# Performance work log

Hardware: AMD Instinct MI355X
Metric: run time of the kernel (lower is better)

The kernel has to match this reference:

```python
import jax, jax.numpy as jnp
import numpy as np

B, C, H, W = 16, 256, 64, 64


def _conv1x1(x, w, b):
    # x: [B,C,H,W], w: [O,C], b: [O]
    return jnp.einsum('oc,bchw->bohw', w, x) + b[None, :, None, None]


def _maxpool2(x):
    b, c, h, w = x.shape
    return x.reshape(b, c, h // 2, 2, w // 2, 2).max(axis=(3, 5))


def setup_inputs() -> dict:
    key = jax.random.key(0)
    ks = jax.random.split(key, 10)
    c8, c2 = C // 8, C // 2
    s = lambda fan_in: 1.0 / np.sqrt(fan_in)
    return {
        'x': jax.random.normal(ks[0], (B, C, H, W), dtype=jnp.float32),
        'query_w': jax.random.normal(ks[1], (c8, C), dtype=jnp.float32) * s(C),
        'query_b': jnp.zeros((c8,), dtype=jnp.float32),
        'key_w': jax.random.normal(ks[2], (c8, C), dtype=jnp.float32) * s(C),
        'key_b': jnp.zeros((c8,), dtype=jnp.float32),
        'val_w': jax.random.normal(ks[3], (c2, C), dtype=jnp.float32) * s(C),
        'val_b': jnp.zeros((c2,), dtype=jnp.float32),
        'val2_w': jax.random.normal(ks[4], (C, c2), dtype=jnp.float32) * s(c2),
        'val2_b': jnp.zeros((C,), dtype=jnp.float32),
        'gamma': jnp.zeros((1,), dtype=jnp.float32) + 0.5,  # nonzero so attention path contributes
    }


def reference(x, query_w, query_b, key_w, key_b, val_w, val_b, val2_w, val2_b, gamma):
    b, nc, h, w = x.shape
    loc = h * w
    down = loc // 4
    c8, c2 = nc // 8, nc // 2

    # query: conv then raw view to [B, HW, C//8] (NOT a permute; faithful to torch .view)
    q = _conv1x1(x, query_w, query_b)              # [B, C/8, H, W]
    q = q.reshape(b, loc, c8)                      # raw reshape, mixes channel/spatial

    # key: conv -> 2x2 maxpool -> raw view -> permute(0,2,1)
    k = _maxpool2(_conv1x1(x, key_w, key_b))       # [B, C/8, H/2, W/2]
    k = k.reshape(b, down, c8).transpose(0, 2, 1)  # [B, C/8, down]

    # value: conv -> 2x2 maxpool -> raw view
    v = _maxpool2(_conv1x1(x, val_w, val_b))       # [B, C/2, H/2, W/2]
    v = v.reshape(b, down, c2)                     # [B, down, C/2]

    attn = jnp.einsum('bqd,bdk->bqk', q, k)        # [B, HW, down], no 1/sqrt(d)
    attn_weights = jax.nn.softmax(attn, axis=1)    # softmax over QUERY axis (dim=1), as in source
    applied = jnp.einsum('bqk,bkc->bqc', attn_weights, v)  # [B, HW, C/2]

    # raw view back to [B, C/2, w, h] (note w,h swapped in source)
    applied = applied.reshape(b, c2, w, h)
    out = _conv1x1(applied, val2_w, val2_b)        # [B, C, w, h]
    return gamma * out + x
```

## Files before the change

### kernel.cpp

```cpp
#include <hip/hip_runtime.h>
#include <hip/hip_bf16.h>


typedef short s8v __attribute__((ext_vector_type(8)));
typedef float f4v __attribute__((ext_vector_type(4)));
typedef unsigned short u16v8 __attribute__((ext_vector_type(8)));
typedef unsigned short u16v4 __attribute__((ext_vector_type(4)));

#define MFMA16(a, b, c) __builtin_amdgcn_mfma_f32_16x16x32_bf16((a), (b), (c), 0, 0, 0)
#define LOG2E 1.4426950408889634f
#define EXP2 __builtin_amdgcn_exp2f

__device__ __forceinline__ unsigned short f2b(float f) {
    __hip_bfloat16 h = __float2bfloat16(f);
    return *reinterpret_cast<unsigned short*>(&h);
}
__device__ __forceinline__ float b2f(unsigned short u) {
    union { unsigned int i; float f; } v; v.i = ((unsigned int)u) << 16; return v.f;
}

__global__ void prep_weights(const float* __restrict__ qw, const float* __restrict__ qb,
                             const float* __restrict__ kw, const float* __restrict__ kb,
                             const float* __restrict__ vw, const float* __restrict__ vb,
                             const float* __restrict__ v2w,
                             unsigned short* __restrict__ wqkv, float* __restrict__ bias,
                             unsigned short* __restrict__ w2b) {
    int i = blockIdx.x * 256 + threadIdx.x;
    if (i < 49152) {
        int r = i >> 8, c = i & 255; float v;
        if (r < 32)       v = qw[r * 256 + c];
        else if (r < 64)  v = kw[(r - 32) * 256 + c] * LOG2E;
        else              v = vw[(r - 64) * 256 + c];
        wqkv[i] = f2b(v);
    } else if (i < 49152 + 32768) {
        int k = i - 49152; w2b[k] = f2b(v2w[k]);
    } else if (i < 49152 + 32768 + 192) {
        int r = i - 49152 - 32768;
        bias[r] = (r < 32) ? qb[r] : (r < 64 ? kb[r - 32] * LOG2E : vb[r - 64]);
    }
}

__global__ __launch_bounds__(256) void qkv_pool(const unsigned short* __restrict__ wqkv,
                                                const float* __restrict__ bias,
                                                const float* __restrict__ x,
                                                unsigned short* __restrict__ qf,
                                                unsigned short* __restrict__ kf,
                                                unsigned short* __restrict__ vf) {
    __shared__ alignas(16) unsigned short xt[32768];
    int b = blockIdx.y, r = blockIdx.x;
    int p0 = r * 128;
    int t = threadIdx.x;
    int wave = t >> 6, lane = t & 63;
    int m = lane & 15, quad = lane >> 4;
    const float* xb = x + (size_t)b * 1048576;

    {
        int pq = t & 31, kb = t >> 5;
        #pragma unroll
        for (int s = 0; s < 8; ++s) {
            int kbase = s * 32 + kb * 4;
            float4 f0 = *(const float4*)(xb + (size_t)(kbase + 0) * 4096 + p0 + pq * 4);
            float4 f1 = *(const float4*)(xb + (size_t)(kbase + 1) * 4096 + p0 + pq * 4);
            float4 f2 = *(const float4*)(xb + (size_t)(kbase + 2) * 4096 + p0 + pq * 4);
            float4 f3 = *(const float4*)(xb + (size_t)(kbase + 3) * 4096 + p0 + pq * 4);
            int ko = kbase >> 3, sub = kbase & 7;
            #pragma unroll
            for (int pi = 0; pi < 4; ++pi) {
                int p = pq * 4 + pi;
                float a0 = pi == 0 ? f0.x : pi == 1 ? f0.y : pi == 2 ? f0.z : f0.w;
                float a1 = pi == 0 ? f1.x : pi == 1 ? f1.y : pi == 2 ? f1.z : f1.w;
                float a2 = pi == 0 ? f2.x : pi == 1 ? f2.y : pi == 2 ? f2.z : f2.w;
                float a3 = pi == 0 ? f3.x : pi == 1 ? f3.y : pi == 2 ? f3.z : f3.w;
                u16v4 pk; pk[0] = f2b(a0); pk[1] = f2b(a1); pk[2] = f2b(a2); pk[3] = f2b(a3);
                int swz = (p & 7) ^ ((p >> 2) & 7);
                *(u16v4*)(&xt[p * 256 + ((ko ^ swz) << 3) + sub]) = pk;
            }
        }
    }
    __syncthreads();

    f4v acc[3][8] = {};
    for (int ks = 0; ks < 8; ++ks) {
        int k0 = ks * 32 + quad * 8;
        s8v afr[3];
        for (int mt = 0; mt < 3; ++mt)
            afr[mt] = *(const s8v*)(wqkv + (wave * 48 + mt * 16 + m) * 256 + k0);
        for (int nt = 0; nt < 8; ++nt) {
            int p = nt * 16 + m;
            int swz = (p & 7) ^ ((p >> 2) & 7);
            s8v bfr = *(const s8v*)(&xt[p * 256 + (((ks * 4 + quad) ^ swz) << 3)]);
            for (int mt = 0; mt < 3; ++mt)
                acc[mt][nt] = MFMA16(afr[mt], bfr, acc[mt][nt]);
        }
    }
    for (int mt = 0; mt < 3; ++mt) {
        int obase = wave * 48 + mt * 16;
        if (obase < 32) {
            for (int reg = 0; reg < 4; ++reg) {
                int o = obase + quad * 4 + reg;
                float bi = bias[o];
                for (int nt = 0; nt < 8; ++nt)
                    qf[(size_t)b * 131072 + (size_t)o * 4096 + p0 + nt * 16 + m] =
                        f2b(acc[mt][nt][reg] + bi);
            }
        } else {
            for (int reg = 0; reg < 4; ++reg) {
                int o = obase + quad * 4 + reg;
                float bi = bias[o];
                for (int nt = 0; nt < 4; ++nt) {
                    float vv = fmaxf(acc[mt][nt][reg], acc[mt][nt + 4][reg]);
                    float ov = __shfl_xor(vv, 1);
                    if ((m & 1) == 0) {
                        float res = fmaxf(vv, ov) + bi;
                        int w2 = nt * 8 + (m >> 1);
                        int sp = r * 32 + w2;
                        if (o < 64) kf[(size_t)b * 32768 + (size_t)(o - 32) * 1024 + sp] = f2b(res);
                        else        vf[(size_t)b * 131072 + (size_t)(o - 64) * 1024 + sp] = f2b(res);
                    }
                }
            }
        }
    }
}

__global__ __launch_bounds__(256) void col_stats(const unsigned short* __restrict__ qf,
                                                 const unsigned short* __restrict__ kf,
                                                 float* __restrict__ rs) {
    __shared__ float red[4][32];
    int b = blockIdx.y, j0 = blockIdx.x * 32;
    int wave = threadIdx.x >> 6, lane = threadIdx.x & 63;
    int m = lane & 15, quad = lane >> 4;
    const unsigned short* qb = qf + (size_t)b * 131072;
    f4v zero = {0.f, 0.f, 0.f, 0.f};

    s8v kfr0 = *(const s8v*)(kf + (size_t)b * 32768 + (size_t)(j0 + m) * 32 + quad * 8);
    s8v kfr1 = *(const s8v*)(kf + (size_t)b * 32768 + (size_t)(j0 + 16 + m) * 32 + quad * 8);

    float sm0 = 0.f, sm1 = 0.f;
    for (int it = wave; it < 256; it += 4) {
        s8v afr = *(const s8v*)(qb + (size_t)(it * 16 + m) * 32 + quad * 8);
        f4v s0 = MFMA16(afr, kfr0, zero);
        f4v s1 = MFMA16(afr, kfr1, zero);
        sm0 += (EXP2(s0[0]) + EXP2(s0[1])) + (EXP2(s0[2]) + EXP2(s0[3]));
        sm1 += (EXP2(s1[0]) + EXP2(s1[1])) + (EXP2(s1[2]) + EXP2(s1[3]));
    }
    sm0 += __shfl_xor(sm0, 16); sm0 += __shfl_xor(sm0, 32);
    sm1 += __shfl_xor(sm1, 16); sm1 += __shfl_xor(sm1, 32);
    if (lane < 16) { red[wave][m] = sm0; red[wave][16 + m] = sm1; }
    __syncthreads();
    if (threadIdx.x < 32) {
        float S = (red[0][threadIdx.x] + red[1][threadIdx.x]) +
                  (red[2][threadIdx.x] + red[3][threadIdx.x]);
        rs[b * 1024 + j0 + threadIdx.x] = 1.0f / S;
    }
}

__global__ __launch_bounds__(256) void transpose_scale_v(const unsigned short* __restrict__ src,
                                                         const float* __restrict__ rs,
                                                         unsigned short* __restrict__ dst) {
    __shared__ float tile[64][65];
    int b = blockIdx.z;
    size_t base = (size_t)b * 131072;
    int r0 = blockIdx.x * 64, c0 = blockIdx.y * 64;
    int tr = threadIdx.x >> 6, tc = threadIdx.x & 63;
    float scale = rs[b * 1024 + r0 + tc];
    for (int i = 0; i < 16; ++i) {
        int rl = i * 4 + tr;
        tile[rl][tc] = b2f(src[base + (size_t)(r0 + rl) * 128 + c0 + tc]);
    }
    __syncthreads();
    for (int i = 0; i < 16; ++i) {
        int cl = i * 4 + tr;
        int c = c0 + cl;
        int j = r0 + tc;
        int jc = j >> 7, jl = j & 127, g = jl >> 3, e = jl & 7;
        dst[base + jc * 16384 + c * 128 + ((g ^ (c & 7)) << 3) + e] =
            f2b(tile[tc][cl] * scale);
    }
}

__global__ __launch_bounds__(512, 4) void attn_fused(const unsigned short* __restrict__ qf,
                                                     const unsigned short* __restrict__ kf,
                                                     const unsigned short* __restrict__ vsw,
                                                     unsigned short* __restrict__ fa) {
    __shared__ alignas(16) unsigned short VS[16384];
    __shared__ alignas(16) unsigned short PT[16384];
    int lin = blockIdx.x + (blockIdx.y << 5);
    int b = lin & 15, l0 = (lin >> 4) << 7;
    int tid = threadIdx.x;
    int wave = tid >> 6, lane = tid & 63;
    int m = lane & 15, quad = lane >> 4;
    int ls = wave * 16;
    const unsigned short* qb = qf + (size_t)b * 131072;
    const unsigned short* kb = kf + (size_t)b * 32768;
    const unsigned short* vb = vsw + (size_t)b * 131072;

    s8v qa = *(const s8v*)(qb + (size_t)(l0 + ls + m) * 32 + quad * 8);
    f4v acc[8] = {};
    f4v zero = {0.f, 0.f, 0.f, 0.f};

    for (int jc = 0; jc < 8; ++jc) {
        const unsigned short* src = vb + jc * 16384 + tid * 8;
        u16v8 t0 = *(const u16v8*)(src);
        u16v8 t1 = *(const u16v8*)(src + 4096);
        u16v8 t2 = *(const u16v8*)(src + 8192);
        u16v8 t3 = *(const u16v8*)(src + 12288);

        int j0 = jc * 128;
        int l = ls + m;
        for (int jt = 0; jt < 8; ++jt) {
            s8v kfr = *(const s8v*)(kb + (size_t)(j0 + jt * 16 + m) * 32 + quad * 8);
            f4v st = MFMA16(kfr, qa, zero);
            unsigned int u0 = ((unsigned)f2b(EXP2(st[1])) << 16) |
                              (unsigned)f2b(EXP2(st[0]));
            unsigned int u1 = ((unsigned)f2b(EXP2(st[3])) << 16) |
                              (unsigned)f2b(EXP2(st[2]));
            int g = jt * 2 + (quad >> 1);
            int sub = (quad & 1) * 4;
            uint2 uu; uu.x = u0; uu.y = u1;
            *(uint2*)(&PT[l * 128 + ((g ^ (l & 7)) << 3) + sub]) = uu;
        }

        __syncthreads();

        {
            unsigned short* dstl = VS + tid * 8;
            *(u16v8*)(dstl)         = t0;
            *(u16v8*)(dstl + 4096)  = t1;
            *(u16v8*)(dstl + 8192)  = t2;
            *(u16v8*)(dstl + 12288) = t3;
        }

        __syncthreads();

        __builtin_amdgcn_s_setprio(1);
        for (int ks = 0; ks < 4; ++ks) {
            int gp = ks * 4 + quad;
            s8v pa = *(const s8v*)(&PT[l * 128 + ((gp ^ (l & 7)) << 3)]);
            for (int ct = 0; ct < 8; ++ct) {
                int c = ct * 16 + m;
                s8v vfr = *(const s8v*)(&VS[c * 128 + ((gp ^ (c & 7)) << 3)]);
                acc[ct] = MFMA16(pa, vfr, acc[ct]);
            }
        }
        __builtin_amdgcn_s_setprio(0);
    }
    for (int ct = 0; ct < 8; ++ct)
        for (int reg = 0; reg < 4; ++reg) {
            int l = l0 + ls + quad * 4 + reg;
            fa[(size_t)b * 524288 + (size_t)l * 128 + ct * 16 + m] = f2b(acc[ct][reg]);
        }
}

__global__ __launch_bounds__(256, 4) void final_gemm(const unsigned short* __restrict__ w2b,
                                                     const float* __restrict__ v2b,
                                                     const float* __restrict__ gamma,
                                                     const unsigned short* __restrict__ fa,
                                                     const float* __restrict__ x,
                                                     float* __restrict__ out) {
    __shared__ alignas(16) unsigned short gt[64][136];
    int b = blockIdx.z, bx = blockIdx.x;
    int p0 = bx * 64;
    int page = bx >> 1;
    int c0 = (bx & 1) * 64;
    int wave = threadIdx.x >> 6, lane = threadIdx.x & 63;
    int m = lane & 15, quad = lane >> 4;
    int obase = blockIdx.y * 128 + wave * 32;

    int row  = threadIdx.x >> 1;
    int half = threadIdx.x & 1;
    const unsigned short* fr = fa + (size_t)b * 524288 +
                               (size_t)(row * 32 + page) * 128 + c0 + half * 32;
    u16v8 t0 = *(const u16v8*)(fr);
    u16v8 t1 = *(const u16v8*)(fr + 8);
    u16v8 t2 = *(const u16v8*)(fr + 16);
    u16v8 t3 = *(const u16v8*)(fr + 24);

    float4 xv[2][4];
    #pragma unroll
    for (int mt = 0; mt < 2; ++mt) {
        size_t xrow = (size_t)b * 1048576 + (size_t)(obase + mt * 16 + m) * 4096;
        #pragma unroll
        for (int nt = 0; nt < 4; ++nt)
            xv[mt][nt] = *(const float4*)(x + xrow + p0 + nt * 16 + quad * 4);
    }

    {
        int pb = half * 32;
        #pragma unroll
        for (int i = 0; i < 8; ++i) {
            gt[pb + i][row]      = t0[i];
            gt[pb + 8 + i][row]  = t1[i];
            gt[pb + 16 + i][row] = t2[i];
            gt[pb + 24 + i][row] = t3[i];
        }
    }
    __syncthreads();

    f4v acc[2][4] = {};
    for (int ks = 0; ks < 4; ++ks) {
        int k0 = ks * 32 + quad * 8;
        s8v afr[2], bfr[4];
        #pragma unroll
        for (int mt = 0; mt < 2; ++mt)
            afr[mt] = *(const s8v*)(w2b + (obase + mt * 16 + m) * 128 + k0);
        #pragma unroll
        for (int nt = 0; nt < 4; ++nt)
            bfr[nt] = *(const s8v*)(&gt[nt * 16 + m][k0]);
        #pragma unroll
        for (int mt = 0; mt < 2; ++mt)
            #pragma unroll
            for (int nt = 0; nt < 4; ++nt)
                acc[mt][nt] = MFMA16(bfr[nt], afr[mt], acc[mt][nt]);
    }
    float g = gamma[0];
    #pragma unroll
    for (int mt = 0; mt < 2; ++mt) {
        int o = obase + mt * 16 + m;
        float bi = v2b[o];
        size_t xrow = (size_t)b * 1048576 + (size_t)o * 4096;
        #pragma unroll
        for (int nt = 0; nt < 4; ++nt) {
            size_t xi = xrow + p0 + nt * 16 + quad * 4;
            float4 ov;
            ov.x = g * (acc[mt][nt][0] + bi) + xv[mt][nt].x;
            ov.y = g * (acc[mt][nt][1] + bi) + xv[mt][nt].y;
            ov.z = g * (acc[mt][nt][2] + bi) + xv[mt][nt].z;
            ov.w = g * (acc[mt][nt][3] + bi) + xv[mt][nt].w;
            *(float4*)(out + xi) = ov;
        }
    }
}

extern "C" void kernel_launch(void* const* d_in, const int* in_sizes, int n_in,
                              void* d_out, int out_size, void* d_ws, size_t ws_size,
                              hipStream_t stream) {
    const float* x    = (const float*)d_in[0];
    const float* qw   = (const float*)d_in[1];
    const float* qb   = (const float*)d_in[2];
    const float* kw   = (const float*)d_in[3];
    const float* kb   = (const float*)d_in[4];
    const float* vw   = (const float*)d_in[5];
    const float* vb   = (const float*)d_in[6];
    const float* v2w  = (const float*)d_in[7];
    const float* v2b  = (const float*)d_in[8];
    const float* gamma = (const float*)d_in[9];
    float* out = (float*)d_out;

    char* ws = (char*)d_ws;
    size_t off = 0;
    auto alloc = [&](size_t bytes) { size_t o = off; off = (off + bytes + 255) & ~(size_t)255; return o; };
    unsigned short* wqkv = (unsigned short*)(ws + alloc(192 * 256 * 2));
    unsigned short* w2b  = (unsigned short*)(ws + alloc(256 * 128 * 2));
    float*          bias = (float*)(ws + alloc(192 * 4));
    float*          rs   = (float*)(ws + alloc((size_t)16 * 1024 * 4));
    unsigned short* qf   = (unsigned short*)(ws + alloc((size_t)16 * 131072 * 2));
    unsigned short* kf   = (unsigned short*)(ws + alloc((size_t)16 * 32768 * 2));
    unsigned short* vf   = (unsigned short*)(ws + alloc((size_t)16 * 131072 * 2));
    unsigned short* vt   = (unsigned short*)(ws + alloc((size_t)16 * 131072 * 2));
    unsigned short* fa   = (unsigned short*)(ws + alloc((size_t)16 * 524288 * 2));
    (void)ws_size; (void)in_sizes; (void)n_in; (void)out_size;

    prep_weights<<<321, 256, 0, stream>>>(qw, qb, kw, kb, vw, vb, v2w, wqkv, bias, w2b);
    qkv_pool<<<dim3(32, 16), 256, 0, stream>>>(wqkv, bias, x, qf, kf, vf);
    col_stats<<<dim3(32, 16), 256, 0, stream>>>(qf, kf, rs);
    transpose_scale_v<<<dim3(16, 2, 16), 256, 0, stream>>>(vf, rs, vt);
    attn_fused<<<dim3(32, 16), 512, 0, stream>>>(qf, kf, vt, fa);
    final_gemm<<<dim3(64, 2, 16), 256, 0, stream>>>(w2b, v2b, gamma, fa, x, out);
}
```

Baseline: 220.1 us.

## Fuse column stats with V scale-transpose and halve P tile in attention

The column-sum kernel now also scales and transposes its 32 rows of V into the swizzled layout, using the reciprocals kept in shared memory. This drops the separate transpose kernel and the global rs buffer. The attention kernel splits each 128-key chunk into two 64-key halves, so the P staging buffer in LDS is half as large. That may allow more resident blocks, and the exp work of the second half can interleave with MFMA work. The cost is an extra exp/MFMA phase per chunk, and the transposed V writes are now 8-element gathers from shared memory.

```diff
diff --git a/kernel.cpp b/kernel.cpp
--- a/kernel.cpp
+++ b/kernel.cpp
@@ -123,10 +123,13 @@
     }
 }
 
-__global__ __launch_bounds__(256) void col_stats(const unsigned short* __restrict__ qf,
-                                                 const unsigned short* __restrict__ kf,
-                                                 float* __restrict__ rs) {
+__global__ __launch_bounds__(256) void col_stats_scale(const unsigned short* __restrict__ qf,
+                                                       const unsigned short* __restrict__ kf,
+                                                       const unsigned short* __restrict__ vf,
+                                                       unsigned short* __restrict__ vt) {
     __shared__ float red[4][32];
+    __shared__ float rsl[32];
+    __shared__ unsigned short vtile[32][136];
     int b = blockIdx.y, j0 = blockIdx.x * 32;
     int wave = threadIdx.x >> 6, lane = threadIdx.x & 63;
     int m = lane & 15, quad = lane >> 4;
@@ -151,31 +154,35 @@
     if (threadIdx.x < 32) {
         float S = (red[0][threadIdx.x] + red[1][threadIdx.x]) +
                   (red[2][threadIdx.x] + red[3][threadIdx.x]);
-        rs[b * 1024 + j0 + threadIdx.x] = 1.0f / S;
-    }
-}
-
-__global__ __launch_bounds__(256) void transpose_scale_v(const unsigned short* __restrict__ src,
-                                                         const float* __restrict__ rs,
-                                                         unsigned short* __restrict__ dst) {
-    __shared__ float tile[64][65];
-    int b = blockIdx.z;
-    size_t base = (size_t)b * 131072;
-    int r0 = blockIdx.x * 64, c0 = blockIdx.y * 64;
-    int tr = threadIdx.x >> 6, tc = threadIdx.x & 63;
-    float scale = rs[b * 1024 + r0 + tc];
-    for (int i = 0; i < 16; ++i) {
-        int rl = i * 4 + tr;
-        tile[rl][tc] = b2f(src[base + (size_t)(r0 + rl) * 128 + c0 + tc]);
-    }
-    __syncthreads();
-    for (int i = 0; i < 16; ++i) {
-        int cl = i * 4 + tr;
-        int c = c0 + cl;
-        int j = r0 + tc;
-        int jc = j >> 7, jl = j & 127, g = jl >> 3, e = jl & 7;
-        dst[base + jc * 16384 + c * 128 + ((g ^ (c & 7)) << 3) + e] =
-            f2b(tile[tc][cl] * scale);
+        rsl[threadIdx.x] = 1.0f / S;
+    }
+    __syncthreads();
+
+    const unsigned short* vfb = vf + (size_t)b * 131072;
+    #pragma unroll
+    for (int r2 = 0; r2 < 2; ++r2) {
+        int qq = threadIdx.x + r2 * 256;
+        int j = qq >> 4, c8 = qq & 15;
+        u16v8 v = *(const u16v8*)(vfb + (size_t)(j0 + j) * 128 + c8 * 8);
+        float sc = rsl[j];
+        u16v8 o;
+        #pragma unroll
+        for (int i = 0; i < 8; ++i) o[i] = f2b(b2f((unsigned short)v[i]) * sc);
+        *(u16v8*)(&vtile[j][c8 * 8]) = o;
+    }
+    __syncthreads();
+
+    unsigned short* vtb = vt + (size_t)b * 131072;
+    int jc = j0 >> 7, gbase = (j0 & 127) >> 3;
+    #pragma unroll
+    for (int r2 = 0; r2 < 2; ++r2) {
+        int qq = threadIdx.x + r2 * 256;
+        int c = qq >> 2, gi = qq & 3;
+        int g = gbase + gi;
+        u16v8 o;
+        #pragma unroll
+        for (int e = 0; e < 8; ++e) o[e] = vtile[gi * 8 + e][c];
+        *(u16v8*)(vtb + jc * 16384 + c * 128 + ((g ^ (c & 7)) << 3)) = o;
     }
 }
 
@@ -184,7 +191,7 @@
                                                      const unsigned short* __restrict__ vsw,
                                                      unsigned short* __restrict__ fa) {
     __shared__ alignas(16) unsigned short VS[16384];
-    __shared__ alignas(16) unsigned short PT[16384];
+    __shared__ alignas(16) unsigned short PT[8192];
     int lin = blockIdx.x + (blockIdx.y << 5);
     int b = lin & 15, l0 = (lin >> 4) << 7;
     int tid = threadIdx.x;
@@ -198,6 +205,7 @@
     s8v qa = *(const s8v*)(qb + (size_t)(l0 + ls + m) * 32 + quad * 8);
     f4v acc[8] = {};
     f4v zero = {0.f, 0.f, 0.f, 0.f};
+    int l = ls + m;
 
     for (int jc = 0; jc < 8; ++jc) {
         const unsigned short* src = vb + jc * 16384 + tid * 8;
@@ -207,18 +215,15 @@
         u16v8 t3 = *(const u16v8*)(src + 12288);
 
         int j0 = jc * 128;
-        int l = ls + m;
-        for (int jt = 0; jt < 8; ++jt) {
+        for (int jt = 0; jt < 4; ++jt) {
             s8v kfr = *(const s8v*)(kb + (size_t)(j0 + jt * 16 + m) * 32 + quad * 8);
             f4v st = MFMA16(kfr, qa, zero);
-            unsigned int u0 = ((unsigned)f2b(EXP2(st[1])) << 16) |
-                              (unsigned)f2b(EXP2(st[0]));
-            unsigned int u1 = ((unsigned)f2b(EXP2(st[3])) << 16) |
-                              (unsigned)f2b(EXP2(st[2]));
+            unsigned int u0 = ((unsigned)f2b(EXP2(st[1])) << 16) | (unsigned)f2b(EXP2(st[0]));
+            unsigned int u1 = ((unsigned)f2b(EXP2(st[3])) << 16) | (unsigned)f2b(EXP2(st[2]));
             int g = jt * 2 + (quad >> 1);
             int sub = (quad & 1) * 4;
             uint2 uu; uu.x = u0; uu.y = u1;
-            *(uint2*)(&PT[l * 128 + ((g ^ (l & 7)) << 3) + sub]) = uu;
+            *(uint2*)(&PT[l * 64 + ((g ^ (l & 7)) << 3) + sub]) = uu;
         }
 
         __syncthreads();
@@ -234,9 +239,9 @@
         __syncthreads();
 
         __builtin_amdgcn_s_setprio(1);
-        for (int ks = 0; ks < 4; ++ks) {
+        for (int ks = 0; ks < 2; ++ks) {
             int gp = ks * 4 + quad;
-            s8v pa = *(const s8v*)(&PT[l * 128 + ((gp ^ (l & 7)) << 3)]);
+            s8v pa = *(const s8v*)(&PT[l * 64 + ((gp ^ (l & 7)) << 3)]);
             for (int ct = 0; ct < 8; ++ct) {
                 int c = ct * 16 + m;
                 s8v vfr = *(const s8v*)(&VS[c * 128 + ((gp ^ (c & 7)) << 3)]);
@@ -244,11 +249,35 @@
             }
         }
         __builtin_amdgcn_s_setprio(0);
+
+        for (int jt = 4; jt < 8; ++jt) {
+            s8v kfr = *(const s8v*)(kb + (size_t)(j0 + jt * 16 + m) * 32 + quad * 8);
+            f4v st = MFMA16(kfr, qa, zero);
+            unsigned int u0 = ((unsigned)f2b(EXP2(st[1])) << 16) | (unsigned)f2b(EXP2(st[0]));
+            unsigned int u1 = ((unsigned)f2b(EXP2(st[3])) << 16) | (unsigned)f2b(EXP2(st[2]));
+            int g = (jt - 4) * 2 + (quad >> 1);
+            int sub = (quad & 1) * 4;
+            uint2 uu; uu.x = u0; uu.y = u1;
+            *(uint2*)(&PT[l * 64 + ((g ^ (l & 7)) << 3) + sub]) = uu;
+        }
+
+        __builtin_amdgcn_s_setprio(1);
+        for (int ks = 0; ks < 2; ++ks) {
+            int gp = ks * 4 + quad;
+            s8v pa = *(const s8v*)(&PT[l * 64 + ((gp ^ (l & 7)) << 3)]);
+            int gv = 8 + gp;
+            for (int ct = 0; ct < 8; ++ct) {
+                int c = ct * 16 + m;
+                s8v vfr = *(const s8v*)(&VS[c * 128 + ((gv ^ (c & 7)) << 3)]);
+                acc[ct] = MFMA16(pa, vfr, acc[ct]);
+            }
+        }
+        __builtin_amdgcn_s_setprio(0);
     }
     for (int ct = 0; ct < 8; ++ct)
         for (int reg = 0; reg < 4; ++reg) {
-            int l = l0 + ls + quad * 4 + reg;
-            fa[(size_t)b * 524288 + (size_t)l * 128 + ct * 16 + m] = f2b(acc[ct][reg]);
+            int lo = l0 + ls + quad * 4 + reg;
+            fa[(size_t)b * 524288 + (size_t)lo * 128 + ct * 16 + m] = f2b(acc[ct][reg]);
         }
 }
 
@@ -353,7 +382,6 @@
     unsigned short* wqkv = (unsigned short*)(ws + alloc(192 * 256 * 2));
     unsigned short* w2b  = (unsigned short*)(ws + alloc(256 * 128 * 2));
     float*          bias = (float*)(ws + alloc(192 * 4));
-    float*          rs   = (float*)(ws + alloc((size_t)16 * 1024 * 4));
     unsigned short* qf   = (unsigned short*)(ws + alloc((size_t)16 * 131072 * 2));
     unsigned short* kf   = (unsigned short*)(ws + alloc((size_t)16 * 32768 * 2));
     unsigned short* vf   = (unsigned short*)(ws + alloc((size_t)16 * 131072 * 2));
@@ -363,8 +391,7 @@
 
     prep_weights<<<321, 256, 0, stream>>>(qw, qb, kw, kb, vw, vb, v2w, wqkv, bias, w2b);
     qkv_pool<<<dim3(32, 16), 256, 0, stream>>>(wqkv, bias, x, qf, kf, vf);
-    col_stats<<<dim3(32, 16), 256, 0, stream>>>(qf, kf, rs);
-    transpose_scale_v<<<dim3(16, 2, 16), 256, 0, stream>>>(vf, rs, vt);
+    col_stats_scale<<<dim3(32, 16), 256, 0, stream>>>(qf, kf, vf, vt);
     attn_fused<<<dim3(32, 16), 512, 0, stream>>>(qf, kf, vt, fa);
     final_gemm<<<dim3(64, 2, 16), 256, 0, stream>>>(w2b, v2b, gamma, fa, x, out);
 }
```

Result: faster. 215.3 us (median of 2 runs) (-2.2%).
